# Kernel tuning notes

Measured on AMD Instinct MI355X. Metric: run time of the kernel, lower is better.

## Reference

```python
import jax, jax.numpy as jnp
import numpy as np

B, S, D = 1, 2048, 2048
HQ, HKV, HD = 32, 8, 64
EXPAND = HQ // HKV

def _rotate_half(x):
    x1, x2 = x[..., : x.shape[-1] // 2], x[..., x.shape[-1] // 2 :]
    return jnp.concatenate((-x2, x1), axis=-1)

def setup_inputs() -> dict:
    key = jax.random.key(0)
    k1, k2, k3 = jax.random.split(key, 3)
    hidden_states = jax.random.normal(k1, (B, S, D), dtype=jnp.float32)
    # Llama weight init scale ~ small
    Wq = jax.random.normal(k2, (HQ * HD, D), dtype=jnp.float32) * 0.02
    Wk = jax.random.normal(k3, (HKV * HD, D), dtype=jnp.float32) * 0.02
    # true rotary cos/sin tables, shape [B, S, HD]
    inv_freq = 1.0 / (10000.0 ** (jnp.arange(0, HD, 2, dtype=jnp.float32) / HD))
    pos = jnp.arange(S, dtype=jnp.float32)
    freqs = pos[:, None] * inv_freq[None, :]            # [S, HD/2]
    emb = jnp.concatenate((freqs, freqs), axis=-1)       # [S, HD]
    cos = jnp.broadcast_to(jnp.cos(emb)[None], (B, S, HD))
    sin = jnp.broadcast_to(jnp.sin(emb)[None], (B, S, HD))
    attn_mask = jnp.zeros((B, 1, S, S), dtype=jnp.float32)  # accepted but unused by the module
    return {"hidden_states": hidden_states, "cos": cos, "sin": sin,
            "attn_mask": attn_mask, "Wq": Wq, "Wk": Wk}

def reference(hidden_states, cos, sin, attn_mask, Wq, Wk):
    b, s, _ = hidden_states.shape
    # projections (nn.Linear, no bias): x @ W.T
    q = hidden_states @ Wq.T                              # [b, s, HQ*HD]
    k = hidden_states @ Wk.T                              # [b, s, HKV*HD]
    q = q.reshape(b, s, HQ, HD).transpose(0, 2, 1, 3)     # [b, HQ, s, HD]
    k = k.reshape(b, s, HKV, HD).transpose(0, 2, 1, 3)    # [b, HKV, s, HD]
    c = cos[:, None, :, :]                                # unsqueeze_dim=1
    sn = sin[:, None, :, :]
    q = q * c + _rotate_half(q) * sn
    k = k * c + _rotate_half(k) * sn
    k = jnp.repeat(k, EXPAND, axis=1)                     # GQA repeat_interleave -> [b, HQ, s, HD]
    scores = jnp.einsum('bhqd,bhkd->bhqk', q, k)          # NO 1/sqrt(d) scaling (faithful)
    return jax.nn.softmax(scores, axis=-1)
```

## Files before the change

### kernel.cpp

```cpp
#include <hip/hip_runtime.h>
#include <hip/hip_bf16.h>

typedef _Float16 half8 __attribute__((ext_vector_type(8)));
typedef float floatx4 __attribute__((ext_vector_type(4)));

#define SEQ 2048
#define DIM 2048
#define HQ 32
#define HKV 8
#define HD 64
#define NQ (HQ*HD)
#define NK (HKV*HD)
#define NTOT (NQ+NK)
#define LOG2E 1.44269504088896340736f

#define GLOAD_LDS16(g, l) \
    __builtin_amdgcn_global_load_lds( \
        (const __attribute__((address_space(1))) void*)(g), \
        (__attribute__((address_space(3))) void*)(l), 16, 0, 0)

__global__ __launch_bounds__(256) void convert_kernel(
    const float* __restrict__ X, const float* __restrict__ Wq,
    const float* __restrict__ Wk, _Float16* __restrict__ Xh,
    _Float16* __restrict__ Wh)
{
    const long c   = (long)blockIdx.x * 256 + threadIdx.x;
    const long nxc = (long)SEQ * DIM / 8;
    const float* src;
    _Float16* dst;
    if (c < nxc) {
        src = X + c * 8;
        dst = Xh + c * 8;
    } else {
        long f = (c - nxc) * 8;
        src = (f < (long)NQ * DIM) ? Wq + f : Wk + (f - (long)NQ * DIM);
        dst = Wh + f;
    }
    float4 a = ((const float4*)src)[0];
    float4 b = ((const float4*)src)[1];
    half8 h = {(_Float16)a.x, (_Float16)a.y, (_Float16)a.z, (_Float16)a.w,
               (_Float16)b.x, (_Float16)b.y, (_Float16)b.z, (_Float16)b.w};
    *(half8*)dst = h;
}

__global__ __launch_bounds__(256) void gemm1_kernel(
    const _Float16* __restrict__ Xh, const _Float16* __restrict__ Wh,
    const float* __restrict__ cosb, const float* __restrict__ sinb,
    _Float16* __restrict__ qout, _Float16* __restrict__ kout)
{
    __shared__ __align__(16) _Float16 lsA[128 * 64];
    __shared__ __align__(16) _Float16 lsB[128 * 64];
    const int tid  = threadIdx.x;
    const int lane = tid & 63;
    const int wv   = tid >> 6;
    const int wm   = wv & 1, wn = wv >> 1;
    const int m    = lane & 15, quad = lane >> 4;
    const int s0   = blockIdx.x * 128;
    const int n0   = blockIdx.y * 128;

    floatx4 acc[4][4];
    #pragma unroll
    for (int i = 0; i < 4; i++)
        #pragma unroll
        for (int j = 0; j < 4; j++)
            acc[i][j] = floatx4{0.f, 0.f, 0.f, 0.f};

    for (int k0 = 0; k0 < DIM; k0 += 64) {
        __syncthreads();
        #pragma unroll
        for (int r = 0; r < 4; r++) {
            int c    = r * 256 + tid;
            int row  = c >> 3;
            int chg  = (c & 7) ^ (row & 7);
            GLOAD_LDS16(Xh + (long)(s0 + row) * DIM + k0 + chg * 8,
                        (char*)lsA + (r * 256 + wv * 64) * 16);
        }
        #pragma unroll
        for (int r = 0; r < 4; r++) {
            int c    = r * 256 + tid;
            int row  = c >> 3;
            int chg  = (c & 7) ^ (row & 7);
            GLOAD_LDS16(Wh + (long)(n0 + row) * DIM + k0 + chg * 8,
                        (char*)lsB + (r * 256 + wv * 64) * 16);
        }
        __syncthreads();

        #pragma unroll
        for (int kk = 0; kk < 2; kk++) {
            half8 aF[4], bF[4];
            const int pc = ((kk << 2) | quad) ^ (m & 7);
            #pragma unroll
            for (int i = 0; i < 4; i++)
                aF[i] = *(const half8*)(lsA + (wm * 64 + i * 16 + m) * 64 + pc * 8);
            #pragma unroll
            for (int j = 0; j < 4; j++)
                bF[j] = *(const half8*)(lsB + (wn * 64 + j * 16 + m) * 64 + pc * 8);
            #pragma unroll
            for (int i = 0; i < 4; i++)
                #pragma unroll
                for (int j = 0; j < 4; j++)
                    acc[i][j] = __builtin_amdgcn_mfma_f32_16x16x32_f16(
                        aF[i], bF[j], acc[i][j], 0, 0, 0);
        }
    }

    #pragma unroll
    for (int i = 0; i < 4; i++) {
        #pragma unroll
        for (int reg = 0; reg < 4; reg++) {
            int s = s0 + wm * 64 + i * 16 + quad * 4 + reg;
            #pragma unroll
            for (int j = 0; j < 4; j++) {
                int col = n0 + wn * 64 + j * 16 + m;
                int d   = j * 16 + m;
                float v = acc[i][j][reg];
                float partner = (j < 2) ? -acc[i][j + 2][reg] : acc[i][j - 2][reg];
                float cs = cosb[s * HD + d];
                float sn = sinb[s * HD + d];
                float o  = v * cs + partner * sn;
                if (col < NQ) {
                    int hq = col >> 6;
                    qout[((long)hq * SEQ + s) * HD + d] = (_Float16)(o * LOG2E);
                } else {
                    int hk = (col - NQ) >> 6;
                    kout[((long)hk * SEQ + s) * HD + d] = (_Float16)o;
                }
            }
        }
    }
}

__global__ __launch_bounds__(512, 2) void attn_kernel(
    const _Float16* __restrict__ qf, const _Float16* __restrict__ kf,
    float* __restrict__ out)
{
    __shared__ float lsT[8][16][256];
    float* redm = &lsT[0][0][0];
    float* redl = redm + 256;

    const int tid  = threadIdx.x;
    const int lane = tid & 63;
    const int w    = tid >> 6;
    const int m    = lane & 15, quad = lane >> 4;
    const int qb   = blockIdx.x;
    const int h    = blockIdx.y;
    const int kvh  = h >> 2;
    const int s0   = qb * 32;

    const _Float16* qbase = qf + ((long)h * SEQ + s0) * HD;
    const _Float16* kbase = kf + (long)kvh * SEQ * HD;

    half8 bQ[2][2];
    #pragma unroll
    for (int g = 0; g < 2; g++) {
        bQ[g][0] = *(const half8*)(qbase + (long)(g * 16 + m) * HD + quad * 8);
        bQ[g][1] = *(const half8*)(qbase + (long)(g * 16 + m) * HD + 32 + quad * 8);
    }

    floatx4 acc[2][16];
    const _Float16* kp = kbase + (long)(w * 256 + m) * HD + quad * 8;
    half8 aK0 = *(const half8*)(kp);
    half8 aK1 = *(const half8*)(kp + 32);
    #pragma unroll
    for (int ct = 0; ct < 16; ct++) {
        half8 nK0, nK1;
        if (ct < 15) {
            const _Float16* np = kbase + (long)(w * 256 + (ct + 1) * 16 + m) * HD + quad * 8;
            nK0 = *(const half8*)(np);
            nK1 = *(const half8*)(np + 32);
        }
        #pragma unroll
        for (int g = 0; g < 2; g++) {
            floatx4 a = floatx4{0.f, 0.f, 0.f, 0.f};
            a = __builtin_amdgcn_mfma_f32_16x16x32_f16(aK0, bQ[g][0], a, 0, 0, 0);
            a = __builtin_amdgcn_mfma_f32_16x16x32_f16(aK1, bQ[g][1], a, 0, 0, 0);
            acc[g][ct] = a;
        }
        aK0 = nK0;
        aK1 = nK1;
    }

    float gmax[2];
    #pragma unroll
    for (int g = 0; g < 2; g++) {
        float lm = acc[g][0][0];
        #pragma unroll
        for (int ct = 0; ct < 16; ct++)
            #pragma unroll
            for (int r = 0; r < 4; r++) lm = fmaxf(lm, acc[g][ct][r]);
        lm = fmaxf(lm, __shfl_xor(lm, 16));
        lm = fmaxf(lm, __shfl_xor(lm, 32));
        if (quad == 0) redm[(g * 8 + w) * 16 + m] = lm;
    }
    __syncthreads();
    #pragma unroll
    for (int g = 0; g < 2; g++) {
        float gm = redm[(g * 8 + 0) * 16 + m];
        #pragma unroll
        for (int ww = 1; ww < 8; ww++)
            gm = fmaxf(gm, redm[(g * 8 + ww) * 16 + m]);
        gmax[g] = gm;
    }

    float inv_[2];
    #pragma unroll
    for (int g = 0; g < 2; g++) {
        float ls = 0.f;
        #pragma unroll
        for (int ct = 0; ct < 16; ct++) {
            #pragma unroll
            for (int r = 0; r < 4; r++) {
                float e = exp2f(acc[g][ct][r] - gmax[g]);
                acc[g][ct][r] = e;
                ls += e;
            }
        }
        ls += __shfl_xor(ls, 16);
        ls += __shfl_xor(ls, 32);
        if (quad == 0) redl[(g * 8 + w) * 16 + m] = ls;
    }
    __syncthreads();
    #pragma unroll
    for (int g = 0; g < 2; g++) {
        float tot = 0.f;
        #pragma unroll
        for (int ww = 0; ww < 8; ww++) tot += redl[(g * 8 + ww) * 16 + m];
        inv_[g] = 1.0f / tot;
    }
    __syncthreads();

    #pragma unroll
    for (int g = 0; g < 2; g++) {
        #pragma unroll
        for (int ct = 0; ct < 16; ct++) {
            floatx4 v = acc[g][ct];
            v[0] *= inv_[g]; v[1] *= inv_[g]; v[2] *= inv_[g]; v[3] *= inv_[g];
            int slot = (ct * 4 + quad) ^ m;
            *(floatx4*)&lsT[w][m][slot * 4] = v;
        }
        #pragma unroll
        for (int r = 0; r < 16; r++) {
            int slot = lane ^ r;
            floatx4 v = *(const floatx4*)&lsT[w][r][slot * 4];
            float* dst = out + ((long)h * SEQ + s0 + g * 16 + r) * SEQ
                             + w * 256 + lane * 4;
            __builtin_nontemporal_store(v, (floatx4*)dst);
        }
    }
}

extern "C" void kernel_launch(void* const* d_in, const int* in_sizes, int n_in,
                              void* d_out, int out_size, void* d_ws, size_t ws_size,
                              hipStream_t stream) {
    const float* hidden = (const float*)d_in[0];
    const float* cosb   = (const float*)d_in[1];
    const float* sinb   = (const float*)d_in[2];
    const float* Wq     = (const float*)d_in[4];
    const float* Wk     = (const float*)d_in[5];
    float* out = (float*)d_out;

    char* ws = (char*)d_ws;
    _Float16* Xh = (_Float16*)ws;
    _Float16* Wh = (_Float16*)(ws + 8388608);
    _Float16* qf = (_Float16*)(ws + 8388608 + 10485760);
    _Float16* kf = (_Float16*)(ws + 8388608 + 10485760 + 8388608);

    convert_kernel<<<4608, 256, 0, stream>>>(hidden, Wq, Wk, Xh, Wh);
    gemm1_kernel<<<dim3(16, 20), 256, 0, stream>>>(Xh, Wh, cosb, sinb, qf, kf);
    attn_kernel<<<dim3(64, 32), 512, 0, stream>>>(qf, kf, out);
}
```

Measured before the change: 677.4 us.

## Fuse convert, projection GEMM and attention into one cooperative persistent kernel

```diff
diff --git a/kernel.cpp b/kernel.cpp
--- a/kernel.cpp
+++ b/kernel.cpp
@@ -1,5 +1,8 @@
 #include <hip/hip_runtime.h>
+#include <hip/hip_cooperative_groups.h>
 #include <hip/hip_bf16.h>
+
+namespace cg = cooperative_groups;
 
 typedef _Float16 half8 __attribute__((ext_vector_type(8)));
 typedef float floatx4 __attribute__((ext_vector_type(4)));
@@ -19,232 +22,238 @@
         (const __attribute__((address_space(1))) void*)(g), \
         (__attribute__((address_space(3))) void*)(l), 16, 0, 0)
 
-__global__ __launch_bounds__(256) void convert_kernel(
-    const float* __restrict__ X, const float* __restrict__ Wq,
-    const float* __restrict__ Wk, _Float16* __restrict__ Xh,
-    _Float16* __restrict__ Wh)
+__global__ __launch_bounds__(512, 2) void fused_kernel(
+    const float* __restrict__ X, const float* __restrict__ cosb,
+    const float* __restrict__ sinb, const float* __restrict__ Wq,
+    const float* __restrict__ Wk, float* __restrict__ out,
+    _Float16* __restrict__ Xh, _Float16* __restrict__ Wh,
+    _Float16* __restrict__ qf, _Float16* __restrict__ kf)
 {
-    const long c   = (long)blockIdx.x * 256 + threadIdx.x;
-    const long nxc = (long)SEQ * DIM / 8;
-    const float* src;
-    _Float16* dst;
-    if (c < nxc) {
-        src = X + c * 8;
-        dst = Xh + c * 8;
-    } else {
-        long f = (c - nxc) * 8;
-        src = (f < (long)NQ * DIM) ? Wq + f : Wk + (f - (long)NQ * DIM);
-        dst = Wh + f;
-    }
-    float4 a = ((const float4*)src)[0];
-    float4 b = ((const float4*)src)[1];
-    half8 h = {(_Float16)a.x, (_Float16)a.y, (_Float16)a.z, (_Float16)a.w,
-               (_Float16)b.x, (_Float16)b.y, (_Float16)b.z, (_Float16)b.w};
-    *(half8*)dst = h;
-}
-
-__global__ __launch_bounds__(256) void gemm1_kernel(
-    const _Float16* __restrict__ Xh, const _Float16* __restrict__ Wh,
-    const float* __restrict__ cosb, const float* __restrict__ sinb,
-    _Float16* __restrict__ qout, _Float16* __restrict__ kout)
-{
-    __shared__ __align__(16) _Float16 lsA[128 * 64];
-    __shared__ __align__(16) _Float16 lsB[128 * 64];
+    __shared__ __align__(16) float lsT[8][16][256];
+    cg::grid_group grid = cg::this_grid();
     const int tid  = threadIdx.x;
+    const int bid  = blockIdx.x;
     const int lane = tid & 63;
     const int wv   = tid >> 6;
-    const int wm   = wv & 1, wn = wv >> 1;
     const int m    = lane & 15, quad = lane >> 4;
-    const int s0   = blockIdx.x * 128;
-    const int n0   = blockIdx.y * 128;
-
-    floatx4 acc[4][4];
-    #pragma unroll
-    for (int i = 0; i < 4; i++)
-        #pragma unroll
-        for (int j = 0; j < 4; j++)
-            acc[i][j] = floatx4{0.f, 0.f, 0.f, 0.f};
-
-    for (int k0 = 0; k0 < DIM; k0 += 64) {
-        __syncthreads();
-        #pragma unroll
-        for (int r = 0; r < 4; r++) {
-            int c    = r * 256 + tid;
-            int row  = c >> 3;
-            int chg  = (c & 7) ^ (row & 7);
-            GLOAD_LDS16(Xh + (long)(s0 + row) * DIM + k0 + chg * 8,
-                        (char*)lsA + (r * 256 + wv * 64) * 16);
-        }
-        #pragma unroll
-        for (int r = 0; r < 4; r++) {
-            int c    = r * 256 + tid;
-            int row  = c >> 3;
-            int chg  = (c & 7) ^ (row & 7);
-            GLOAD_LDS16(Wh + (long)(n0 + row) * DIM + k0 + chg * 8,
-                        (char*)lsB + (r * 256 + wv * 64) * 16);
-        }
-        __syncthreads();
-
-        #pragma unroll
-        for (int kk = 0; kk < 2; kk++) {
-            half8 aF[4], bF[4];
-            const int pc = ((kk << 2) | quad) ^ (m & 7);
-            #pragma unroll
-            for (int i = 0; i < 4; i++)
-                aF[i] = *(const half8*)(lsA + (wm * 64 + i * 16 + m) * 64 + pc * 8);
-            #pragma unroll
-            for (int j = 0; j < 4; j++)
-                bF[j] = *(const half8*)(lsB + (wn * 64 + j * 16 + m) * 64 + pc * 8);
-            #pragma unroll
-            for (int i = 0; i < 4; i++)
-                #pragma unroll
-                for (int j = 0; j < 4; j++)
-                    acc[i][j] = __builtin_amdgcn_mfma_f32_16x16x32_f16(
-                        aF[i], bF[j], acc[i][j], 0, 0, 0);
+
+    {
+        const long nxc  = (long)SEQ * DIM / 8;
+        const long nall = nxc + (long)NTOT * DIM / 8;
+        for (long c = (long)bid * 512 + tid; c < nall; c += 131072) {
+            const float* src; _Float16* dst;
+            if (c < nxc) { src = X + c * 8; dst = Xh + c * 8; }
+            else {
+                long f = (c - nxc) * 8;
+                src = (f < (long)NQ * DIM) ? Wq + f : Wk + (f - (long)NQ * DIM);
+                dst = Wh + f;
+            }
+            float4 a = ((const float4*)src)[0];
+            float4 b = ((const float4*)src)[1];
+            half8 h = {(_Float16)a.x, (_Float16)a.y, (_Float16)a.z, (_Float16)a.w,
+                       (_Float16)b.x, (_Float16)b.y, (_Float16)b.z, (_Float16)b.w};
+            *(half8*)dst = h;
         }
     }
-
-    #pragma unroll
-    for (int i = 0; i < 4; i++) {
-        #pragma unroll
-        for (int reg = 0; reg < 4; reg++) {
-            int s = s0 + wm * 64 + i * 16 + quad * 4 + reg;
-            #pragma unroll
-            for (int j = 0; j < 4; j++) {
-                int col = n0 + wn * 64 + j * 16 + m;
-                int d   = j * 16 + m;
-                float v = acc[i][j][reg];
-                float partner = (j < 2) ? -acc[i][j + 2][reg] : acc[i][j - 2][reg];
-                float cs = cosb[s * HD + d];
-                float sn = sinb[s * HD + d];
-                float o  = v * cs + partner * sn;
-                if (col < NQ) {
-                    int hq = col >> 6;
-                    qout[((long)hq * SEQ + s) * HD + d] = (_Float16)(o * LOG2E);
-                } else {
-                    int hk = (col - NQ) >> 6;
-                    kout[((long)hk * SEQ + s) * HD + d] = (_Float16)o;
+    __threadfence();
+    grid.sync();
+
+    {
+        _Float16* lsA = (_Float16*)&lsT[0][0][0];
+        _Float16* lsB = lsA + 128 * 64;
+        const int wm = wv >> 1;
+        const int wn = wv & 1;
+        for (int t = bid; t < 320; t += 256) {
+            const int s0 = (t & 15) * 128;
+            const int n0 = (t >> 4) * 128;
+            floatx4 acc[2][4];
+            #pragma unroll
+            for (int i = 0; i < 2; i++)
+                #pragma unroll
+                for (int j = 0; j < 4; j++)
+                    acc[i][j] = floatx4{0.f, 0.f, 0.f, 0.f};
+
+            for (int k0 = 0; k0 < DIM; k0 += 64) {
+                __syncthreads();
+                #pragma unroll
+                for (int r = 0; r < 2; r++) {
+                    int c   = r * 512 + tid;
+                    int row = c >> 3;
+                    int chg = (c & 7) ^ (row & 7);
+                    GLOAD_LDS16(Xh + (long)(s0 + row) * DIM + k0 + chg * 8,
+                                (char*)lsA + (r * 512 + wv * 64) * 16);
+                }
+                #pragma unroll
+                for (int r = 0; r < 2; r++) {
+                    int c   = r * 512 + tid;
+                    int row = c >> 3;
+                    int chg = (c & 7) ^ (row & 7);
+                    GLOAD_LDS16(Wh + (long)(n0 + row) * DIM + k0 + chg * 8,
+                                (char*)lsB + (r * 512 + wv * 64) * 16);
+                }
+                __syncthreads();
+
+                #pragma unroll
+                for (int kk = 0; kk < 2; kk++) {
+                    half8 aF[2], bF[4];
+                    const int pc = ((kk << 2) | quad) ^ (m & 7);
+                    #pragma unroll
+                    for (int i = 0; i < 2; i++)
+                        aF[i] = *(const half8*)(lsA + (wm * 32 + i * 16 + m) * 64 + pc * 8);
+                    #pragma unroll
+                    for (int j = 0; j < 4; j++)
+                        bF[j] = *(const half8*)(lsB + (wn * 64 + j * 16 + m) * 64 + pc * 8);
+                    #pragma unroll
+                    for (int i = 0; i < 2; i++)
+                        #pragma unroll
+                        for (int j = 0; j < 4; j++)
+                            acc[i][j] = __builtin_amdgcn_mfma_f32_16x16x32_f16(
+                                aF[i], bF[j], acc[i][j], 0, 0, 0);
+                }
+            }
+
+            #pragma unroll
+            for (int i = 0; i < 2; i++) {
+                #pragma unroll
+                for (int reg = 0; reg < 4; reg++) {
+                    int s = s0 + wm * 32 + i * 16 + quad * 4 + reg;
+                    #pragma unroll
+                    for (int j = 0; j < 4; j++) {
+                        int col = n0 + wn * 64 + j * 16 + m;
+                        int d   = j * 16 + m;
+                        float v = acc[i][j][reg];
+                        float partner = (j < 2) ? -acc[i][j + 2][reg] : acc[i][j - 2][reg];
+                        float cs = cosb[s * HD + d];
+                        float sn = sinb[s * HD + d];
+                        float o  = v * cs + partner * sn;
+                        if (col < NQ) {
+                            int hq = col >> 6;
+                            qf[((long)hq * SEQ + s) * HD + d] = (_Float16)(o * LOG2E);
+                        } else {
+                            int hk = (col - NQ) >> 6;
+                            kf[((long)hk * SEQ + s) * HD + d] = (_Float16)o;
+                        }
+                    }
                 }
             }
         }
     }
-}
-
-__global__ __launch_bounds__(512, 2) void attn_kernel(
-    const _Float16* __restrict__ qf, const _Float16* __restrict__ kf,
-    float* __restrict__ out)
-{
-    __shared__ float lsT[8][16][256];
-    float* redm = &lsT[0][0][0];
-    float* redl = redm + 256;
-
-    const int tid  = threadIdx.x;
-    const int lane = tid & 63;
-    const int w    = tid >> 6;
-    const int m    = lane & 15, quad = lane >> 4;
-    const int qb   = blockIdx.x;
-    const int h    = blockIdx.y;
-    const int kvh  = h >> 2;
-    const int s0   = qb * 32;
-
-    const _Float16* qbase = qf + ((long)h * SEQ + s0) * HD;
-    const _Float16* kbase = kf + (long)kvh * SEQ * HD;
-
-    half8 bQ[2][2];
-    #pragma unroll
-    for (int g = 0; g < 2; g++) {
-        bQ[g][0] = *(const half8*)(qbase + (long)(g * 16 + m) * HD + quad * 8);
-        bQ[g][1] = *(const half8*)(qbase + (long)(g * 16 + m) * HD + 32 + quad * 8);
-    }
-
-    floatx4 acc[2][16];
-    const _Float16* kp = kbase + (long)(w * 256 + m) * HD + quad * 8;
-    half8 aK0 = *(const half8*)(kp);
-    half8 aK1 = *(const half8*)(kp + 32);
-    #pragma unroll
-    for (int ct = 0; ct < 16; ct++) {
-        half8 nK0, nK1;
-        if (ct < 15) {
-            const _Float16* np = kbase + (long)(w * 256 + (ct + 1) * 16 + m) * HD + quad * 8;
-            nK0 = *(const half8*)(np);
-            nK1 = *(const half8*)(np + 32);
-        }
-        #pragma unroll
-        for (int g = 0; g < 2; g++) {
-            floatx4 a = floatx4{0.f, 0.f, 0.f, 0.f};
-            a = __builtin_amdgcn_mfma_f32_16x16x32_f16(aK0, bQ[g][0], a, 0, 0, 0);
-            a = __builtin_amdgcn_mfma_f32_16x16x32_f16(aK1, bQ[g][1], a, 0, 0, 0);
-            acc[g][ct] = a;
-        }
-        aK0 = nK0;
-        aK1 = nK1;
-    }
-
-    float gmax[2];
-    #pragma unroll
-    for (int g = 0; g < 2; g++) {
-        float lm = acc[g][0][0];
-        #pragma unroll
-        for (int ct = 0; ct < 16; ct++)
-            #pragma unroll
-            for (int r = 0; r < 4; r++) lm = fmaxf(lm, acc[g][ct][r]);
-        lm = fmaxf(lm, __shfl_xor(lm, 16));
-        lm = fmaxf(lm, __shfl_xor(lm, 32));
-        if (quad == 0) redm[(g * 8 + w) * 16 + m] = lm;
-    }
-    __syncthreads();
-    #pragma unroll
-    for (int g = 0; g < 2; g++) {
-        float gm = redm[(g * 8 + 0) * 16 + m];
-        #pragma unroll
-        for (int ww = 1; ww < 8; ww++)
-            gm = fmaxf(gm, redm[(g * 8 + ww) * 16 + m]);
-        gmax[g] = gm;
-    }
-
-    float inv_[2];
-    #pragma unroll
-    for (int g = 0; g < 2; g++) {
-        float ls = 0.f;
-        #pragma unroll
-        for (int ct = 0; ct < 16; ct++) {
-            #pragma unroll
-            for (int r = 0; r < 4; r++) {
-                float e = exp2f(acc[g][ct][r] - gmax[g]);
-                acc[g][ct][r] = e;
-                ls += e;
-            }
-        }
-        ls += __shfl_xor(ls, 16);
-        ls += __shfl_xor(ls, 32);
-        if (quad == 0) redl[(g * 8 + w) * 16 + m] = ls;
-    }
-    __syncthreads();
-    #pragma unroll
-    for (int g = 0; g < 2; g++) {
-        float tot = 0.f;
-        #pragma unroll
-        for (int ww = 0; ww < 8; ww++) tot += redl[(g * 8 + ww) * 16 + m];
-        inv_[g] = 1.0f / tot;
-    }
-    __syncthreads();
-
-    #pragma unroll
-    for (int g = 0; g < 2; g++) {
-        #pragma unroll
-        for (int ct = 0; ct < 16; ct++) {
-            floatx4 v = acc[g][ct];
-            v[0] *= inv_[g]; v[1] *= inv_[g]; v[2] *= inv_[g]; v[3] *= inv_[g];
-            int slot = (ct * 4 + quad) ^ m;
-            *(floatx4*)&lsT[w][m][slot * 4] = v;
-        }
-        #pragma unroll
-        for (int r = 0; r < 16; r++) {
-            int slot = lane ^ r;
-            floatx4 v = *(const floatx4*)&lsT[w][r][slot * 4];
-            float* dst = out + ((long)h * SEQ + s0 + g * 16 + r) * SEQ
-                             + w * 256 + lane * 4;
-            __builtin_nontemporal_store(v, (floatx4*)dst);
+    __threadfence();
+    grid.sync();
+
+    {
+        float* redm = &lsT[0][0][0];
+        float* redl = redm + 256;
+        const int w = wv;
+
+        for (int u = 0; u < 8; u++) {
+            __syncthreads();
+            const int unit = u * 256 + bid;
+            const int qb   = unit & 63;
+            const int h    = unit >> 6;
+            const int kvh  = h >> 2;
+            const int s0   = qb * 32;
+
+            const _Float16* qbase = qf + ((long)h * SEQ + s0) * HD;
+            const _Float16* kbase = kf + (long)kvh * SEQ * HD;
+
+            half8 bQ[2][2];
+            #pragma unroll
+            for (int g = 0; g < 2; g++) {
+                bQ[g][0] = *(const half8*)(qbase + (long)(g * 16 + m) * HD + quad * 8);
+                bQ[g][1] = *(const half8*)(qbase + (long)(g * 16 + m) * HD + 32 + quad * 8);
+            }
+
+            floatx4 acc[2][16];
+            const _Float16* kp = kbase + (long)(w * 256 + m) * HD + quad * 8;
+            half8 aK0 = *(const half8*)(kp);
+            half8 aK1 = *(const half8*)(kp + 32);
+            #pragma unroll
+            for (int ct = 0; ct < 16; ct++) {
+                half8 nK0, nK1;
+                if (ct < 15) {
+                    const _Float16* np = kbase + (long)(w * 256 + (ct + 1) * 16 + m) * HD + quad * 8;
+                    nK0 = *(const half8*)(np);
+                    nK1 = *(const half8*)(np + 32);
+                }
+                #pragma unroll
+                for (int g = 0; g < 2; g++) {
+                    floatx4 a = floatx4{0.f, 0.f, 0.f, 0.f};
+                    a = __builtin_amdgcn_mfma_f32_16x16x32_f16(aK0, bQ[g][0], a, 0, 0, 0);
+                    a = __builtin_amdgcn_mfma_f32_16x16x32_f16(aK1, bQ[g][1], a, 0, 0, 0);
+                    acc[g][ct] = a;
+                }
+                aK0 = nK0;
+                aK1 = nK1;
+            }
+
+            float gmax[2];
+            #pragma unroll
+            for (int g = 0; g < 2; g++) {
+                float lm = acc[g][0][0];
+                #pragma unroll
+                for (int ct = 0; ct < 16; ct++)
+                    #pragma unroll
+                    for (int r = 0; r < 4; r++) lm = fmaxf(lm, acc[g][ct][r]);
+                lm = fmaxf(lm, __shfl_xor(lm, 16));
+                lm = fmaxf(lm, __shfl_xor(lm, 32));
+                if (quad == 0) redm[(g * 8 + w) * 16 + m] = lm;
+            }
+            __syncthreads();
+            #pragma unroll
+            for (int g = 0; g < 2; g++) {
+                float gm = redm[(g * 8 + 0) * 16 + m];
+                #pragma unroll
+                for (int ww = 1; ww < 8; ww++)
+                    gm = fmaxf(gm, redm[(g * 8 + ww) * 16 + m]);
+                gmax[g] = gm;
+            }
+
+            float inv_[2];
+            #pragma unroll
+            for (int g = 0; g < 2; g++) {
+                float ls = 0.f;
+                #pragma unroll
+                for (int ct = 0; ct < 16; ct++) {
+                    #pragma unroll
+                    for (int r = 0; r < 4; r++) {
+                        float e = exp2f(acc[g][ct][r] - gmax[g]);
+                        acc[g][ct][r] = e;
+                        ls += e;
+                    }
+                }
+                ls += __shfl_xor(ls, 16);
+                ls += __shfl_xor(ls, 32);
+                if (quad == 0) redl[(g * 8 + w) * 16 + m] = ls;
+            }
+            __syncthreads();
+            #pragma unroll
+            for (int g = 0; g < 2; g++) {
+                float tot = 0.f;
+                #pragma unroll
+                for (int ww = 0; ww < 8; ww++) tot += redl[(g * 8 + ww) * 16 + m];
+                inv_[g] = 1.0f / tot;
+            }
+            __syncthreads();
+
+            #pragma unroll
+            for (int g = 0; g < 2; g++) {
+                #pragma unroll
+                for (int ct = 0; ct < 16; ct++) {
+                    floatx4 v = acc[g][ct];
+                    v[0] *= inv_[g]; v[1] *= inv_[g]; v[2] *= inv_[g]; v[3] *= inv_[g];
+                    int slot = (ct * 4 + quad) ^ m;
+                    *(floatx4*)&lsT[w][m][slot * 4] = v;
+                }
+                #pragma unroll
+                for (int r = 0; r < 16; r++) {
+                    int slot = lane ^ r;
+                    floatx4 v = *(const floatx4*)&lsT[w][r][slot * 4];
+                    float* dst = out + ((long)h * SEQ + s0 + g * 16 + r) * SEQ
+                                     + w * 256 + lane * 4;
+                    __builtin_nontemporal_store(v, (floatx4*)dst);
+                }
+            }
         }
     }
 }
@@ -265,7 +274,9 @@
     _Float16* qf = (_Float16*)(ws + 8388608 + 10485760);
     _Float16* kf = (_Float16*)(ws + 8388608 + 10485760 + 8388608);
 
-    convert_kernel<<<4608, 256, 0, stream>>>(hidden, Wq, Wk, Xh, Wh);
-    gemm1_kernel<<<dim3(16, 20), 256, 0, stream>>>(Xh, Wh, cosb, sinb, qf, kf);
-    attn_kernel<<<dim3(64, 32), 512, 0, stream>>>(qf, kf, out);
+    void* args[] = {(void*)&hidden, (void*)&cosb, (void*)&sinb, (void*)&Wq,
+                    (void*)&Wk, (void*)&out, (void*)&Xh, (void*)&Wh,
+                    (void*)&qf, (void*)&kf};
+    hipLaunchCooperativeKernel((const void*)fused_kernel, dim3(256), dim3(512),
+                               args, 0, stream);
 }
```

New measurement: 878.7 us. 1.3x slower.
